# Kernel tuning notes

Hardware: AMD Instinct MI355X
Metric: run time of the kernel (lower is better)

The kernel has to match this reference:

```python
import jax, jax.numpy as jnp
import numpy as np


def setup_inputs() -> dict:
    key = jax.random.key(0)
    k = jax.random.split(key, 8)
    B, Cin, Cout, H, W, K = 4, 256, 256, 96, 96, 3
    x = jax.random.normal(k[0], (B, Cin, H, W), jnp.float32)
    # offset-predicting 3x3 conv (2*K*K = 18 channels, y/x pairs), near-zero init
    w_off = jax.random.normal(k[1], (2 * K * K, Cin, 3, 3), jnp.float32) * 0.01
    b_off = jnp.zeros((2 * K * K,), jnp.float32)
    w_dcn = jax.random.normal(k[2], (Cout, Cin, K, K), jnp.float32) * (1.0 / np.sqrt(Cin * K * K))
    b_dcn = jnp.zeros((Cout,), jnp.float32)
    gamma = jnp.ones((Cout,), jnp.float32)
    beta = jnp.zeros((Cout,), jnp.float32)
    w2 = jax.random.normal(k[3], (1, Cout, 3, 3), jnp.float32) * (1.0 / np.sqrt(Cout * 9))
    b2 = jnp.zeros((1,), jnp.float32)
    return {"x": x, "w_off": w_off, "b_off": b_off, "w_dcn": w_dcn, "b_dcn": b_dcn,
            "gamma": gamma, "beta": beta, "w2": w2, "b2": b2}


def _conv2d(x, w, b, pad):
    y = jax.lax.conv_general_dilated(x, w, (1, 1), [(pad, pad), (pad, pad)],
                                     dimension_numbers=("NCHW", "OIHW", "NCHW"))
    return y + b[None, :, None, None]


def _deform_conv(x, offsets, w, b):
    # deform_conv2d v1 (stride 1, dilation 1, padding 1, 1 offset group)
    B, Cin, H, W = x.shape
    Cout, _, K, _ = w.shape
    K2 = K * K
    pad = 1
    off = offsets.reshape(B, K2, 2, H, W)  # (y, x) pairs per kernel tap
    ky = (jnp.arange(K2) // K).astype(x.dtype) - pad
    kx = (jnp.arange(K2) % K).astype(x.dtype) - pad
    base_y = jnp.arange(H, dtype=x.dtype)[None, None, :, None] + ky[None, :, None, None]
    base_x = jnp.arange(W, dtype=x.dtype)[None, None, None, :] + kx[None, :, None, None]
    py = base_y + off[:, :, 0]  # [B,K2,H,W]
    px = base_x + off[:, :, 1]

    def sample(img, py, px):  # img [Cin,H,W]; py/px [K2,H,W]
        y0f = jnp.floor(py); x0f = jnp.floor(px)
        wy = py - y0f; wx = px - x0f
        y0 = y0f.astype(jnp.int32); x0 = x0f.astype(jnp.int32)

        def gather(yi, xi):
            valid = ((yi >= 0) & (yi < H) & (xi >= 0) & (xi < W)).astype(img.dtype)
            v = img[:, jnp.clip(yi, 0, H - 1), jnp.clip(xi, 0, W - 1)]  # [Cin,K2,H,W]
            return v * valid[None]

        return (gather(y0, x0) * ((1 - wy) * (1 - wx))[None]
                + gather(y0, x0 + 1) * ((1 - wy) * wx)[None]
                + gather(y0 + 1, x0) * (wy * (1 - wx))[None]
                + gather(y0 + 1, x0 + 1) * (wy * wx)[None])

    sampled = jax.vmap(sample)(x, py, px)  # [B,Cin,K2,H,W]
    out = jnp.einsum("bikhw,oik->bohw", sampled, w.reshape(Cout, Cin, K2))
    return out + b[None, :, None, None]


def _group_norm(x, gamma, beta, groups=32, eps=1e-5):
    B, C, H, W = x.shape
    xr = x.reshape(B, groups, C // groups, H, W)
    mu = xr.mean(axis=(2, 3, 4), keepdims=True)
    var = xr.var(axis=(2, 3, 4), keepdims=True)
    xn = ((xr - mu) * jax.lax.rsqrt(var + eps)).reshape(B, C, H, W)
    return xn * gamma[None, :, None, None] + beta[None, :, None, None]


def reference(x, w_off, b_off, w_dcn, b_dcn, gamma, beta, w2, b2):
    offsets = _conv2d(x, w_off, b_off, 1)                      # [B,18,H,W]
    x1 = _group_norm(_deform_conv(x, offsets, w_dcn, b_dcn), gamma, beta)
    x_s = jax.nn.sigmoid(_conv2d(x1, w2, b2, 1))               # [B,1,H,W]
    return x1 * x_s
```

## Files before the change

### kernel.cpp

```cpp
#include <hip/hip_runtime.h>
#include <math.h>

#define HW 9216
#define CIN 256
#define COUT 256

typedef _Float16 f16;
typedef _Float16 half8 __attribute__((ext_vector_type(8)));
typedef float f32x4 __attribute__((ext_vector_type(4)));

struct F2 { float a, b; };

__device__ __forceinline__ void swz576(int bx, int& b, int& tile) {
    int xcd = bx & 7, k = bx >> 3;
    b = xcd >> 1;
    tile = (xcd & 1) * 72 + k;
}

__global__ __launch_bounds__(256) void k_prep_x(const float* __restrict__ x,
                                                f16* __restrict__ xt) {
    __shared__ f16 tile[64][256];
    int b, tl; swz576(blockIdx.x, b, tl);
    int pxb = tl * 64;
    int t = threadIdx.x;
    int cq = t >> 2, q = t & 3;
    for (int cp = 0; cp < 4; ++cp) {
        int c = cp * 64 + cq;
        const float* src = x + ((size_t)(b * 256 + c)) * HW + pxb + q * 16;
#pragma unroll
        for (int ii = 0; ii < 4; ++ii) {
            float4 v = *(const float4*)(src + ii * 4);
            int p0 = q * 16 + ii * 4;
            tile[p0 + 0][c] = (f16)v.x; tile[p0 + 1][c] = (f16)v.y;
            tile[p0 + 2][c] = (f16)v.z; tile[p0 + 3][c] = (f16)v.w;
        }
    }
    __syncthreads();
    int cg = t & 31, ph = t >> 5;
#pragma unroll
    for (int it = 0; it < 8; ++it) {
        int px = it * 8 + ph;
        *(uint4*)(xt + ((size_t)(b * HW + pxb + px)) * 256 + cg * 8) =
            *(const uint4*)&tile[px][cg * 8];
    }
}

__global__ __launch_bounds__(256) void k_prep_w(const float* __restrict__ w_dcn,
                                                f16* __restrict__ wt2) {
    int gid = blockIdx.x * 256 + threadIdx.x;
    int e = gid & 7;
    int cout = (gid >> 3) & 255;
    int r2 = gid >> 11;
    int g = r2 & 3, kb = (r2 >> 2) & 7, tap = r2 >> 5;
    int cin = kb * 32 + ((e >> 2) << 4) + (g << 2) + (e & 3);
    wt2[gid] = (f16)w_dcn[((size_t)cout * 256 + cin) * 9 + tap];
}

__global__ __launch_bounds__(256) void k_prep_wo(const float* __restrict__ w_off,
                                                 float* __restrict__ w_offp) {
    int gid = blockIdx.x * 256 + threadIdx.x;
    int cin = gid & 255;
    int r = gid >> 8;
    int tap = r % 9, o = r / 9;
    w_offp[gid] = w_off[((size_t)o * 256 + cin) * 9 + tap];
}

__global__ __launch_bounds__(512) void k_off(const f16* __restrict__ xt,
                                             const float* __restrict__ w_offp,
                                             const float* __restrict__ b_off,
                                             f16* __restrict__ off) {
    __shared__ float red[8][64][19];
    int b, tl; swz576(blockIdx.x, b, tl);
    int t = threadIdx.x;
    int px = t & 63;
    int cpart = __builtin_amdgcn_readfirstlane(t >> 6);
    int pxf = tl * 64 + px;
    int h = pxf / 96, w = pxf - h * 96;
    const char* xb = (const char*)(xt + (size_t)b * HW * 256);

    float acc[18];
#pragma unroll
    for (int o = 0; o < 18; ++o) acc[o] = 0.f;

    for (int tap = 0; tap < 9; ++tap) {
        int dy = tap / 3 - 1, dx = tap - (tap / 3) * 3 - 1;
        int h2 = h + dy, w2 = w + dx;
        bool ok = ((unsigned)h2 < 96u) && ((unsigned)w2 < 96u);
        int src = ok ? h2 * 96 + w2 : 0;
        const char* xp = xb + (size_t)src * 512;
#pragma unroll
        for (int mi = 0; mi < 4; ++mi) {
            int mm = cpart * 4 + mi;
            uint4 raw = *(const uint4*)(xp + mm * 16);
            const f16* hx = (const f16*)&raw;
            float xv[8];
#pragma unroll
            for (int e = 0; e < 8; ++e) xv[e] = ok ? (float)hx[e] : 0.f;
            const float* wb = w_offp + mm * 8;
#pragma unroll
            for (int o = 0; o < 18; ++o) {
                const float* wp = wb + (o * 9 + tap) * 256;
#pragma unroll
                for (int e = 0; e < 8; ++e) acc[o] += wp[e] * xv[e];
            }
        }
    }
#pragma unroll
    for (int o = 0; o < 18; ++o) red[cpart][px][o] = acc[o];
    __syncthreads();
    if (t < 64) {
        float s[18];
#pragma unroll
        for (int o = 0; o < 18; ++o) s[o] = b_off[o];
        for (int cp = 0; cp < 8; ++cp)
#pragma unroll
            for (int o = 0; o < 18; ++o) s[o] += red[cp][t][o];
#pragma unroll
        for (int o = 0; o < 18; ++o)
            off[((size_t)(b * 18 + o)) * HW + tl * 64 + t] = (f16)s[o];
    }
}

__global__ __launch_bounds__(512, 6) void k_dcn(const f16* __restrict__ xt,
                                                const f16* __restrict__ off,
                                                const f16* __restrict__ wt2,
                                                const float* __restrict__ b_dcn,
                                                f16* __restrict__ y,
                                                float* __restrict__ gsum,
                                                float* __restrict__ gss) {
    __shared__ uint4  A4[2048];
    __shared__ int4   idx4[576];
    __shared__ float4 wt4[576];

    int b, tile; swz576(blockIdx.x, b, tile);
    int pxb = tile * 64;
    int t = threadIdx.x;
    int lane = t & 63, wv = t >> 6;

    for (int e = t; e < 576; e += 512) {
        int p = e & 63, tap = e >> 6;
        int pxf = pxb + p;
        int h = pxf / 96, w = pxf - h * 96;
        const f16* ob = off + (size_t)b * 18 * HW + pxf;
        float oy = (float)ob[(size_t)(2 * tap) * HW];
        float ox = (float)ob[(size_t)(2 * tap + 1) * HW];
        float py  = (float)(h + tap / 3 - 1) + oy;
        float pxx = (float)(w + tap % 3 - 1) + ox;
        float y0f = floorf(py), x0f = floorf(pxx);
        float wy = py - y0f, wx = pxx - x0f;
        int yi0 = (int)y0f, xi0 = (int)x0f;
        int yi1 = yi0 + 1, xi1 = xi0 + 1;
        bool vy0 = (unsigned)yi0 < 96u, vy1 = (unsigned)yi1 < 96u;
        bool vx0 = (unsigned)xi0 < 96u, vx1 = (unsigned)xi1 < 96u;
        int cy0 = min(max(yi0, 0), 95), cy1 = min(max(yi1, 0), 95);
        int cx0 = min(max(xi0, 0), 95), cx1 = min(max(xi1, 0), 95);
        idx4[e] = make_int4((cy0 * 96 + cx0) * 512, (cy0 * 96 + cx1) * 512,
                            (cy1 * 96 + cx0) * 512, (cy1 * 96 + cx1) * 512);
        wt4[e] = make_float4((vy0 && vx0) ? (1.f - wy) * (1.f - wx) : 0.f,
                             (vy0 && vx1) ? (1.f - wy) * wx : 0.f,
                             (vy1 && vx0) ? wy * (1.f - wx) : 0.f,
                             (vy1 && vx1) ? wy * wx : 0.f);
    }

    int g = lane >> 4, l15 = lane & 15;
    const char* xtb = (const char*)(xt + (size_t)b * HW * 256);

    f32x4 acc[4][2];
#pragma unroll
    for (int R = 0; R < 4; ++R) {
        acc[R][0] = (f32x4){0.f, 0.f, 0.f, 0.f};
        acc[R][1] = (f32x4){0.f, 0.f, 0.f, 0.f};
    }

    int m = lane & 31;
    int phl = lane >> 5;
    int qq = m & 3;
    int preA_base = (m >> 2) * 64 + (qq & 1) * 32 + ((qq & 2) ? 8 : 0);
    int cout0 = wv * 32 + l15;

    for (int tap = 0; tap < 9; ++tap) {
        __syncthreads();
#pragma unroll
        for (int rr = 0; rr < 4; ++rr) {
            int p = wv * 8 + rr * 2 + phl;
            int4   id  = idx4[tap * 64 + p];
            float4 wgt = wt4[tap * 64 + p];
            uint4 q0 = *(const uint4*)(xtb + id.x + m * 16);
            uint4 q1 = *(const uint4*)(xtb + id.y + m * 16);
            uint4 q2 = *(const uint4*)(xtb + id.z + m * 16);
            uint4 q3 = *(const uint4*)(xtb + id.w + m * 16);
            const f16* a0 = (const f16*)&q0;
            const f16* a1 = (const f16*)&q1;
            const f16* a2 = (const f16*)&q2;
            const f16* a3 = (const f16*)&q3;
            union { f16 h[8]; uint2 u2[2]; } pu;
#pragma unroll
            for (int ii = 0; ii < 8; ++ii) {
                float s = wgt.x * (float)a0[ii] + wgt.y * (float)a1[ii]
                        + wgt.z * (float)a2[ii] + wgt.w * (float)a3[ii];
                pu.h[ii] = (f16)s;
            }
            int preA = p * 512 + preA_base;
            int swz = (p & 7) << 4;
            *(uint2*)((char*)A4 + ((preA) ^ swz))      = pu.u2[0];
            *(uint2*)((char*)A4 + ((preA + 16) ^ swz)) = pu.u2[1];
        }
        __syncthreads();

#pragma unroll
        for (int kb = 0; kb < 8; ++kb) {
            half8 Af[4];
#pragma unroll
            for (int R = 0; R < 4; ++R) {
                int byteA = ((R * 16 + l15) * 512 + kb * 64 + g * 16) ^ ((l15 & 7) << 4);
                Af[R] = *(const half8*)((const char*)A4 + byteA);
            }
#pragma unroll
            for (int nc = 0; nc < 2; ++nc) {
                const f16* bp = wt2 +
                    (((size_t)((tap * 8 + kb) * 4 + g) * 256 + cout0 + nc * 16) << 3);
                half8 Bf = *(const half8*)bp;
#pragma unroll
                for (int R = 0; R < 4; ++R)
                    acc[R][nc] = __builtin_amdgcn_mfma_f32_16x16x32_f16(Af[R], Bf, acc[R][nc], 0, 0, 0);
            }
        }
    }

    float bias0 = b_dcn[cout0], bias1 = b_dcn[cout0 + 16];
    float psum[2] = {0.f, 0.f}, pss[2] = {0.f, 0.f};
    __syncthreads();
    f16* ytile = (f16*)A4;
#pragma unroll
    for (int R = 0; R < 4; ++R)
#pragma unroll
        for (int nc = 0; nc < 2; ++nc) {
            f32x4 v = acc[R][nc];
            float bb = nc ? bias1 : bias0;
            v.x += bb; v.y += bb; v.z += bb; v.w += bb;
            int cout = cout0 + nc * 16;
            int px0 = R * 16 + g * 4;
            ytile[(px0 + 0) * 256 + cout] = (f16)v.x;
            ytile[(px0 + 1) * 256 + cout] = (f16)v.y;
            ytile[(px0 + 2) * 256 + cout] = (f16)v.z;
            ytile[(px0 + 3) * 256 + cout] = (f16)v.w;
            psum[nc] += v.x + v.y + v.z + v.w;
            pss[nc]  += v.x * v.x + v.y * v.y + v.z * v.z + v.w * v.w;
        }
    __syncthreads();
    {
        const uint4* src = (const uint4*)A4;
        uint4* dst = (uint4*)(y + ((size_t)b * HW + pxb) * 256);
#pragma unroll
        for (int i = 0; i < 4; ++i)
            dst[i * 512 + t] = src[i * 512 + t];
    }
    __syncthreads();
    float4* red = (float4*)A4;
    red[t] = make_float4(psum[0], pss[0], psum[1], pss[1]);
    __syncthreads();
    if (t < 32) {
        float s = 0.f, ss = 0.f;
        int wv2 = t >> 2, nc = (t >> 1) & 1, h8 = t & 1;
        for (int g2 = 0; g2 < 4; ++g2)
#pragma unroll
            for (int i = 0; i < 8; ++i) {
                float4 r = red[wv2 * 64 + g2 * 16 + h8 * 8 + i];
                s  += nc ? r.z : r.x;
                ss += nc ? r.w : r.y;
            }
        gsum[((size_t)(b * 32 + t)) * 144 + tile] = s;
        gss [((size_t)(b * 32 + t)) * 144 + tile] = ss;
    }
}

__global__ void k_stats(const float* __restrict__ gsum, const float* __restrict__ gss,
                        const float* __restrict__ gamma, const float* __restrict__ beta,
                        const float* __restrict__ w2,
                        F2* __restrict__ ab, float* __restrict__ w2s) {
    int t = blockIdx.x * 256 + threadIdx.x;
    if (t >= 1024) return;
    int b = t >> 8, c = t & 255, g = c >> 3;
    const float* ps = gsum + (size_t)(b * 32 + g) * 144;
    const float* pq = gss  + (size_t)(b * 32 + g) * 144;
    float s = 0.f, q = 0.f;
    for (int i = 0; i < 144; ++i) { s += ps[i]; q += pq[i]; }
    const float inv_n = 1.f / 73728.f;
    float mu = s * inv_n;
    float var = q * inv_n - mu * mu;
    float rstd = rsqrtf(var + 1e-5f);
    float A = rstd * gamma[c];
    float Bv = beta[c] - mu * A;
    ab[t].a = A;
    ab[t].b = Bv;
#pragma unroll
    for (int tap = 0; tap < 9; ++tap)
        w2s[((size_t)(b * 9 + tap)) * 256 + c] = A * w2[c * 9 + tap];
}

__global__ void k_cb(const F2* __restrict__ ab, const float* __restrict__ w2,
                     float* __restrict__ cB) {
    int t = threadIdx.x;
    if (t >= 36) return;
    int b = t / 9, tap = t - (t / 9) * 9;
    float s = 0.f;
    for (int c = 0; c < 256; ++c) s += ab[b * 256 + c].b * w2[c * 9 + tap];
    cB[t] = s;
}

__global__ __launch_bounds__(256) void k_sig(const f16* __restrict__ y,
                                             const float* __restrict__ w2s,
                                             const float* __restrict__ cB,
                                             const float* __restrict__ b2,
                                             float* __restrict__ sig) {
    __shared__ float red[256][4];
    int bx = blockIdx.x;
    int xcd = bx & 7, kk = bx >> 3;
    int b = xcd >> 1;
    int tile = (xcd & 1) * 72 + (kk >> 1);
    int pxb = tile * 64 + (kk & 1) * 32;
    int t = threadIdx.x;
    int m = t & 31, sub = t >> 5;
    const char* yb = (const char*)(y + (size_t)b * HW * 256);

    int hh[4], ww[4];
#pragma unroll
    for (int rr = 0; rr < 4; ++rr) {
        int pxf = pxb + rr * 8 + sub;
        hh[rr] = pxf / 96; ww[rr] = pxf - hh[rr] * 96;
    }
    float acc[4];
#pragma unroll
    for (int rr = 0; rr < 4; ++rr) acc[rr] = 0.f;

    for (int tap = 0; tap < 9; ++tap) {
        int dy = tap / 3 - 1, dx = tap - (tap / 3) * 3 - 1;
        const float* wp = w2s + ((size_t)(b * 9 + tap)) * 256 + m * 8;
        float wv0[8];
#pragma unroll
        for (int e = 0; e < 8; ++e) wv0[e] = wp[e];
        float cBt = cB[b * 9 + tap];
#pragma unroll
        for (int rr = 0; rr < 4; ++rr) {
            int h2 = hh[rr] + dy, w2i = ww[rr] + dx;
            bool ok = ((unsigned)h2 < 96u) && ((unsigned)w2i < 96u);
            int src = ok ? h2 * 96 + w2i : 0;
            uint4 raw = *(const uint4*)(yb + (size_t)src * 512 + m * 16);
            const f16* hx = (const f16*)&raw;
            float s = 0.f;
#pragma unroll
            for (int e = 0; e < 8; ++e) s += (float)hx[e] * wv0[e];
            s = ok ? s : 0.f;
            if (m == 0 && ok) s += cBt;
            acc[rr] += s;
        }
    }
#pragma unroll
    for (int rr = 0; rr < 4; ++rr) red[t][rr] = acc[rr];
    __syncthreads();
    if (t < 32) {
        int rr = t >> 3, sub2 = t & 7;
        float s = b2[0];
        for (int mm = 0; mm < 32; ++mm) s += red[sub2 * 32 + mm][rr];
        sig[(size_t)b * HW + pxb + rr * 8 + sub2] = 1.f / (1.f + expf(-s));
    }
}

__global__ __launch_bounds__(256) void k_final(const f16* __restrict__ y,
                                               const F2* __restrict__ ab,
                                               const float* __restrict__ sig,
                                               float* __restrict__ out) {
    __shared__ float tile_s[64 * 256];
    int b, tl; swz576(blockIdx.x, b, tl);
    int pxb = tl * 64;
    int t = threadIdx.x;
    int m = t & 31, sub = t >> 5;
    const char* yb = (const char*)(y + ((size_t)b * HW + pxb) * 256);
    float A[8], Bv[8];
    const F2* abp = ab + b * 256 + m * 8;
#pragma unroll
    for (int e = 0; e < 8; ++e) { A[e] = abp[e].a; Bv[e] = abp[e].b; }
#pragma unroll
    for (int rr = 0; rr < 8; ++rr) {
        int px = rr * 8 + sub;
        float sv = sig[(size_t)b * HW + pxb + px];
        uint4 raw = *(const uint4*)(yb + (size_t)px * 512 + m * 16);
        const f16* hx = (const f16*)&raw;
#pragma unroll
        for (int e = 0; e < 8; ++e)
            tile_s[px * 256 + m * 8 + e] = ((float)hx[e] * A[e] + Bv[e]) * sv;
    }
    __syncthreads();
#pragma unroll
    for (int r = 0; r < 16; ++r) {
        int c = r * 16 + (t >> 4);
        int q = t & 15;
        float4 v;
        v.x = tile_s[(q * 4 + 0) * 256 + c];
        v.y = tile_s[(q * 4 + 1) * 256 + c];
        v.z = tile_s[(q * 4 + 2) * 256 + c];
        v.w = tile_s[(q * 4 + 3) * 256 + c];
        *(float4*)(out + ((size_t)(b * 256 + c)) * HW + pxb + q * 4) = v;
    }
}

extern "C" void kernel_launch(void* const* d_in, const int* in_sizes, int n_in,
                              void* d_out, int out_size, void* d_ws, size_t ws_size,
                              hipStream_t stream) {
    (void)in_sizes; (void)n_in; (void)out_size; (void)ws_size;
    const float* x     = (const float*)d_in[0];
    const float* w_off = (const float*)d_in[1];
    const float* b_off = (const float*)d_in[2];
    const float* w_dcn = (const float*)d_in[3];
    const float* b_dcn = (const float*)d_in[4];
    const float* gamma = (const float*)d_in[5];
    const float* beta  = (const float*)d_in[6];
    const float* w2    = (const float*)d_in[7];
    const float* b2    = (const float*)d_in[8];
    float* out = (float*)d_out;

    char* p = (char*)d_ws;
    f16*   offp = (f16*)p;
    f16*   y    = (f16*)(p + 1327104);
    F2*    ab   = (F2*)(p + 20201472);
    char*  xtp  = p + 20209664;
    f16*   xt   = (f16*)xtp;
    f16*   wt2  = (f16*)(p + 39084032);
    char*  wop  = p + 40263680;
    float* w_offp = (float*)wop;
    float* gsum = (float*)wop;
    float* gss  = (float*)(wop + 73728);
    float* w2s  = (float*)xtp;
    float* cB   = (float*)(xtp + 36864);
    float* sig  = (float*)(xtp + 65536);

    k_prep_x <<<576,  256, 0, stream>>>(x, xt);
    k_prep_w <<<2304, 256, 0, stream>>>(w_dcn, wt2);
    k_prep_wo<<<162,  256, 0, stream>>>(w_off, w_offp);
    k_off    <<<576,  512, 0, stream>>>(xt, w_offp, b_off, offp);
    k_dcn    <<<576,  512, 0, stream>>>(xt, offp, wt2, b_dcn, y, gsum, gss);
    k_stats  <<<4,    256, 0, stream>>>(gsum, gss, gamma, beta, w2, ab, w2s);
    k_cb     <<<1,     64, 0, stream>>>(ab, w2, cB);
    k_sig    <<<1152, 256, 0, stream>>>(y, w2s, cB, b2, sig);
    k_final  <<<576,  256, 0, stream>>>(y, ab, sig, out);
}
```

Measured before the change: 499.4 us.

## Prefetch next tap's gather in k_dcn, nontemporal y stores, parallelize k_cb

The deformable-conv kernel now issues the four bilinear-corner global loads for the next tap into registers before the MFMA phase of the current tap, so gather latency overlaps compute. The tap loop is fully unrolled, and the launch-bounds occupancy hint drops from 6 to 4 blocks to leave room for the prefetch registers. The y tile store uses nontemporal stores. k_cb goes from one 36-thread block with serial loops to 36 wavefront blocks doing a shuffle reduction. The risks are extra register pressure and lower occupancy in k_dcn.

New measurement: 527.8 us. +5.7%, slower.

```diff
diff --git a/kernel.cpp b/kernel.cpp
--- a/kernel.cpp
+++ b/kernel.cpp
@@ -8,6 +8,7 @@
 typedef _Float16 f16;
 typedef _Float16 half8 __attribute__((ext_vector_type(8)));
 typedef float f32x4 __attribute__((ext_vector_type(4)));
+typedef unsigned int u32x4 __attribute__((ext_vector_type(4)));
 
 struct F2 { float a, b; };
 
@@ -121,7 +122,7 @@
     }
 }
 
-__global__ __launch_bounds__(512, 6) void k_dcn(const f16* __restrict__ xt,
+__global__ __launch_bounds__(512, 4) void k_dcn(const f16* __restrict__ xt,
                                                 const f16* __restrict__ off,
                                                 const f16* __restrict__ wt2,
                                                 const float* __restrict__ b_dcn,
@@ -178,21 +179,33 @@
     int preA_base = (m >> 2) * 64 + (qq & 1) * 32 + ((qq & 2) ? 8 : 0);
     int cout0 = wv * 32 + l15;
 
-    for (int tap = 0; tap < 9; ++tap) {
-        __syncthreads();
+    uint4 pf[4][4];
+    auto issue_tap = [&](int tp) {
 #pragma unroll
         for (int rr = 0; rr < 4; ++rr) {
             int p = wv * 8 + rr * 2 + phl;
-            int4   id  = idx4[tap * 64 + p];
+            int4 id = idx4[tp * 64 + p];
+            pf[rr][0] = *(const uint4*)(xtb + id.x + m * 16);
+            pf[rr][1] = *(const uint4*)(xtb + id.y + m * 16);
+            pf[rr][2] = *(const uint4*)(xtb + id.z + m * 16);
+            pf[rr][3] = *(const uint4*)(xtb + id.w + m * 16);
+        }
+    };
+
+    __syncthreads();
+    issue_tap(0);
+
+#pragma unroll
+    for (int tap = 0; tap < 9; ++tap) {
+        uint2 cmb[4][2];
+#pragma unroll
+        for (int rr = 0; rr < 4; ++rr) {
+            int p = wv * 8 + rr * 2 + phl;
             float4 wgt = wt4[tap * 64 + p];
-            uint4 q0 = *(const uint4*)(xtb + id.x + m * 16);
-            uint4 q1 = *(const uint4*)(xtb + id.y + m * 16);
-            uint4 q2 = *(const uint4*)(xtb + id.z + m * 16);
-            uint4 q3 = *(const uint4*)(xtb + id.w + m * 16);
-            const f16* a0 = (const f16*)&q0;
-            const f16* a1 = (const f16*)&q1;
-            const f16* a2 = (const f16*)&q2;
-            const f16* a3 = (const f16*)&q3;
+            const f16* a0 = (const f16*)&pf[rr][0];
+            const f16* a1 = (const f16*)&pf[rr][1];
+            const f16* a2 = (const f16*)&pf[rr][2];
+            const f16* a3 = (const f16*)&pf[rr][3];
             union { f16 h[8]; uint2 u2[2]; } pu;
 #pragma unroll
             for (int ii = 0; ii < 8; ++ii) {
@@ -200,10 +213,19 @@
                         + wgt.z * (float)a2[ii] + wgt.w * (float)a3[ii];
                 pu.h[ii] = (f16)s;
             }
+            cmb[rr][0] = pu.u2[0];
+            cmb[rr][1] = pu.u2[1];
+        }
+        if (tap < 8) issue_tap(tap + 1);
+
+        __syncthreads();
+#pragma unroll
+        for (int rr = 0; rr < 4; ++rr) {
+            int p = wv * 8 + rr * 2 + phl;
             int preA = p * 512 + preA_base;
             int swz = (p & 7) << 4;
-            *(uint2*)((char*)A4 + ((preA) ^ swz))      = pu.u2[0];
-            *(uint2*)((char*)A4 + ((preA + 16) ^ swz)) = pu.u2[1];
+            *(uint2*)((char*)A4 + ((preA) ^ swz))      = cmb[rr][0];
+            *(uint2*)((char*)A4 + ((preA + 16) ^ swz)) = cmb[rr][1];
         }
         __syncthreads();
 
@@ -249,11 +271,11 @@
         }
     __syncthreads();
     {
-        const uint4* src = (const uint4*)A4;
-        uint4* dst = (uint4*)(y + ((size_t)b * HW + pxb) * 256);
+        const u32x4* src = (const u32x4*)A4;
+        u32x4* dst = (u32x4*)(y + ((size_t)b * HW + pxb) * 256);
 #pragma unroll
         for (int i = 0; i < 4; ++i)
-            dst[i * 512 + t] = src[i * 512 + t];
+            __builtin_nontemporal_store(src[i * 512 + t], &dst[i * 512 + t]);
     }
     __syncthreads();
     float4* red = (float4*)A4;
@@ -300,12 +322,18 @@
 
 __global__ void k_cb(const F2* __restrict__ ab, const float* __restrict__ w2,
                      float* __restrict__ cB) {
-    int t = threadIdx.x;
-    if (t >= 36) return;
-    int b = t / 9, tap = t - (t / 9) * 9;
+    int bt = blockIdx.x;
+    int b = bt / 9, tap = bt - (bt / 9) * 9;
+    int lane = threadIdx.x;
     float s = 0.f;
-    for (int c = 0; c < 256; ++c) s += ab[b * 256 + c].b * w2[c * 9 + tap];
-    cB[t] = s;
+#pragma unroll
+    for (int i = 0; i < 4; ++i) {
+        int c = i * 64 + lane;
+        s += ab[b * 256 + c].b * w2[c * 9 + tap];
+    }
+#pragma unroll
+    for (int off = 32; off; off >>= 1) s += __shfl_down(s, off);
+    if (lane == 0) cB[bt] = s;
 }
 
 __global__ __launch_bounds__(256) void k_sig(const f16* __restrict__ y,
@@ -440,7 +468,7 @@
     k_off    <<<576,  512, 0, stream>>>(xt, w_offp, b_off, offp);
     k_dcn    <<<576,  512, 0, stream>>>(xt, offp, wt2, b_dcn, y, gsum, gss);
     k_stats  <<<4,    256, 0, stream>>>(gsum, gss, gamma, beta, w2, ab, w2s);
-    k_cb     <<<1,     64, 0, stream>>>(ab, w2, cB);
+    k_cb     <<<36,    64, 0, stream>>>(ab, w2, cB);
     k_sig    <<<1152, 256, 0, stream>>>(y, w2s, cB, b2, sig);
     k_final  <<<576,  256, 0, stream>>>(y, ab, sig, out);
 }
```
